# Performance work log

Measured on AMD Instinct MI355X. Metric: run time of the kernel, lower is better.

Reference implementation:

```python
import jax, jax.numpy as jnp
import numpy as np

DIM = 512
WH, WW = 8, 8
N = WH * WW  # 64 tokens per window
HEADS = 16
HEAD_DIM = DIM // HEADS
SCALE = HEAD_DIM ** -0.5
B_ = 2048
NW = 64  # number of distinct window masks; B_ % NW == 0


def _relative_position_index():
    coords = np.stack(np.meshgrid(np.arange(WH), np.arange(WW), indexing='ij')).reshape(2, -1)  # (2, N)
    rel = coords[:, :, None] - coords[:, None, :]          # (2, N, N)
    rel = rel.transpose(1, 2, 0).astype(np.int64)          # (N, N, 2)
    rel[..., 0] += WH - 1
    rel[..., 1] += WW - 1
    rel[..., 0] *= 2 * WW - 1
    return jnp.asarray(rel.sum(-1))                        # (N, N) in [0, (2Wh-1)(2Ww-1))


def setup_inputs() -> dict:
    key = jax.random.key(0)
    ks = jax.random.split(key, 10)
    q = jax.random.normal(ks[0], (B_, N, DIM), dtype=jnp.float32)
    mask = jax.random.normal(ks[1], (NW, N, N), dtype=jnp.float32)
    s = 0.02
    q_w = jax.random.normal(ks[2], (DIM, DIM), dtype=jnp.float32) * s
    q_b = jnp.zeros((DIM,), dtype=jnp.float32)
    kv_w = jax.random.normal(ks[3], (2 * DIM, DIM), dtype=jnp.float32) * s
    kv_b = jnp.zeros((2 * DIM,), dtype=jnp.float32)
    proj_w = jax.random.normal(ks[4], (DIM, DIM), dtype=jnp.float32) * s
    proj_b = jnp.zeros((DIM,), dtype=jnp.float32)
    bias_table = jax.random.normal(ks[5], ((2 * WH - 1) * (2 * WW - 1), HEADS), dtype=jnp.float32) * s
    rel_index = _relative_position_index()
    return {
        'q': q, 'mask': mask,
        'q_w': q_w, 'q_b': q_b, 'kv_w': kv_w, 'kv_b': kv_b,
        'proj_w': proj_w, 'proj_b': proj_b,
        'bias_table': bias_table, 'rel_index': rel_index,
    }


def reference(q, mask, q_w, q_b, kv_w, kv_b, proj_w, proj_b, bias_table, rel_index):
    Bn, n, c = q.shape
    # q/kv projections (torch Linear: x @ W.T + b)
    qh = (q @ q_w.T + q_b).reshape(Bn, n, HEADS, HEAD_DIM)
    kvh = (q @ kv_w.T + kv_b).reshape(Bn, n, 2, HEADS, HEAD_DIM)
    k = kvh[:, :, 0]  # (B_, N, H, hd)
    v = kvh[:, :, 1]
    # attention scores (B_, H, N, N)
    attn = jnp.einsum('bqhd,bkhd->bhqk', qh * SCALE, k)
    # relative position bias: gather (N*N, H) -> (H, N, N)
    bias = bias_table[rel_index.reshape(-1)].reshape(n, n, HEADS).transpose(2, 0, 1)
    attn = attn + bias[None]
    # shifted-window mask: (nW, N, N) broadcast over batch groups and heads
    nW = mask.shape[0]
    attn = attn.reshape(Bn // nW, nW, HEADS, n, n) + mask[None, :, None]
    attn = attn.reshape(Bn, HEADS, n, n)
    attn = jax.nn.softmax(attn, axis=-1)
    x = jnp.einsum('bhqk,bkhd->bqhd', attn, v).reshape(Bn, n, c)
    x = x @ proj_w.T + proj_b
    return (x, attn)
```

## Files before the change

kernel.cpp:

```cpp
#include <hip/hip_runtime.h>
#include <cstdint>
#include <cstddef>


typedef __bf16 bf16x8 __attribute__((ext_vector_type(8)));
typedef float  f32x4  __attribute__((ext_vector_type(4)));

#define MFMA16(a, b, c) __builtin_amdgcn_mfma_f32_16x16x32_bf16(a, b, c, 0, 0, 0)

__device__ __forceinline__ unsigned short f2bf(float f) {
  unsigned u = __float_as_uint(f);
  u += 0x7fffu + ((u >> 16) & 1u);
  return (unsigned short)(u >> 16);
}

__device__ __forceinline__ void gl2lds16(const void* g, void* l) {
  __builtin_amdgcn_global_load_lds(
      (const __attribute__((address_space(1))) void*)g,
      (__attribute__((address_space(3))) void*)l, 16, 0, 0);
}


__global__ __launch_bounds__(256) void cast_q_k(const float* __restrict__ src,
                                                unsigned short* __restrict__ dst) {
  long idx = (long)blockIdx.x * 256 + threadIdx.x;
  const float4* p = (const float4*)(src + idx * 8);
  float4 a = p[0], b = p[1];
  ushort4 r0 = make_ushort4(f2bf(a.x), f2bf(a.y), f2bf(a.z), f2bf(a.w));
  ushort4 r1 = make_ushort4(f2bf(b.x), f2bf(b.y), f2bf(b.z), f2bf(b.w));
  ushort4* o = (ushort4*)(dst + idx * 8);
  o[0] = r0; o[1] = r1;
}

__global__ __launch_bounds__(256) void pack_w_k(const float* __restrict__ qw,
                                                const float* __restrict__ kvw,
                                                const float* __restrict__ pwsrc,
                                                unsigned short* __restrict__ Wc,
                                                unsigned short* __restrict__ pw,
                                                float scale) {
  int idx = blockIdx.x * 256 + threadIdx.x;
  const float* src;
  unsigned short* dst;
  float s = 1.0f;
  if (idx < 98304) {
    long e = (long)idx * 8;
    int row = (int)(e >> 9);
    int k = (int)(e & 511);
    if (row < 512) { src = qw + (long)row * 512 + k; s = scale; }
    else           { src = kvw + (long)(row - 512) * 512 + k; }
    dst = Wc + e;
  } else {
    long e = (long)(idx - 98304) * 8;
    src = pwsrc + e;
    dst = pw + e;
  }
  float4 a = ((const float4*)src)[0];
  float4 b = ((const float4*)src)[1];
  ushort4 r0 = make_ushort4(f2bf(a.x * s), f2bf(a.y * s), f2bf(a.z * s), f2bf(a.w * s));
  ushort4 r1 = make_ushort4(f2bf(b.x * s), f2bf(b.y * s), f2bf(b.z * s), f2bf(b.w * s));
  ((ushort4*)dst)[0] = r0;
  ((ushort4*)dst)[1] = r1;
}

__global__ __launch_bounds__(256) void prep_misc_k(const float* __restrict__ btab,
                                                   const int* __restrict__ rel,
                                                   const float* __restrict__ qb,
                                                   const float* __restrict__ kvb,
                                                   float* __restrict__ biasF,
                                                   float* __restrict__ bc,
                                                   float scale) {
  int idx = blockIdx.x * 256 + threadIdx.x;
  if (idx < 65536) {
    int ij = idx & 4095;
    int h = idx >> 12;
    biasF[idx] = btab[rel[ij] * 16 + h];
  } else {
    int i = idx - 65536;
    bc[i] = (i < 512) ? qb[i] * scale : kvb[i - 512];
  }
}

template <bool BF16OUT>
__global__ __launch_bounds__(256) void gemm_bt(const unsigned short* __restrict__ A,
                                               const unsigned short* __restrict__ B,
                                               const float* __restrict__ bias,
                                               void* __restrict__ Cp, int N) {
  __shared__ unsigned short As[128 * 64];
  __shared__ unsigned short Bs[128 * 64];
  const int t = threadIdx.x;
  const int lane = t & 63;
  const int wave = t >> 6;
  const int wm = wave >> 1, wn = wave & 1;
  const int quad = lane >> 4, col = lane & 15;
  const long m0 = (long)blockIdx.x * 128;
  const long n0 = (long)blockIdx.y * 128;

  int sidx[4];
  long ga[4], gb[4];
#pragma unroll
  for (int i = 0; i < 4; ++i) {
    int idx = i * 256 + t;
    int r = idx >> 3, cl = idx & 7;
    int cg = cl ^ (r & 7);
    sidx[i] = idx * 8;
    ga[i] = (m0 + r) * 512 + cg * 8;
    gb[i] = (n0 + r) * 512 + cg * 8;
  }

  int offA[2][4], offB[2][4];
#pragma unroll
  for (int mt = 0; mt < 4; ++mt) {
    int rA = wm * 64 + mt * 16 + col;
    int rB = wn * 64 + mt * 16 + col;
#pragma unroll
    for (int ks = 0; ks < 2; ++ks) {
      offA[ks][mt] = rA * 64 + (((ks * 4 + quad) ^ (rA & 7)) * 8);
      offB[ks][mt] = rB * 64 + (((ks * 4 + quad) ^ (rB & 7)) * 8);
    }
  }

  f32x4 acc[4][4];
#pragma unroll
  for (int i = 0; i < 4; ++i)
#pragma unroll
    for (int j = 0; j < 4; ++j) acc[i][j] = (f32x4){0.f, 0.f, 0.f, 0.f};

  for (int kt = 0; kt < 8; ++kt) {
    const unsigned short* Ak = A + kt * 64;
    const unsigned short* Bk = B + kt * 64;
#pragma unroll
    for (int i = 0; i < 4; ++i) gl2lds16(Ak + ga[i], &As[sidx[i]]);
#pragma unroll
    for (int i = 0; i < 4; ++i) gl2lds16(Bk + gb[i], &Bs[sidx[i]]);
    asm volatile("s_waitcnt vmcnt(0)" ::: "memory");
    __syncthreads();
#pragma unroll
    for (int ks = 0; ks < 2; ++ks) {
      bf16x8 af[4], bf[4];
#pragma unroll
      for (int mt = 0; mt < 4; ++mt) af[mt] = *(const bf16x8*)&As[offA[ks][mt]];
#pragma unroll
      for (int nt = 0; nt < 4; ++nt) bf[nt] = *(const bf16x8*)&Bs[offB[ks][nt]];
#pragma unroll
      for (int mt = 0; mt < 4; ++mt)
#pragma unroll
        for (int nt = 0; nt < 4; ++nt)
          acc[mt][nt] = MFMA16(af[mt], bf[nt], acc[mt][nt]);
    }
    __syncthreads();
  }

#pragma unroll
  for (int nt = 0; nt < 4; ++nt) {
    long n = n0 + wn * 64 + nt * 16 + col;
    float bv = bias[n];
#pragma unroll
    for (int mt = 0; mt < 4; ++mt) {
      long mbase = m0 + wm * 64 + mt * 16 + quad * 4;
#pragma unroll
      for (int r = 0; r < 4; ++r) {
        float v = acc[mt][nt][r] + bv;
        long off = (mbase + r) * N + n;
        if (BF16OUT) ((unsigned short*)Cp)[off] = f2bf(v);
        else         ((float*)Cp)[off] = v;
      }
    }
  }
}

__global__ __launch_bounds__(64) void attn_k(const unsigned short* __restrict__ QKV,
                                             const float* __restrict__ mask,
                                             const float* __restrict__ biasF,
                                             float* __restrict__ attn_out,
                                             unsigned short* __restrict__ xh) {
  __shared__ unsigned short Plds[64 * 72];
  __shared__ unsigned short Vt[32 * 72];
  const int bh = blockIdx.x;
  const int b = bh >> 4, h = bh & 15;
  const int lane = threadIdx.x;
  const int quad = lane >> 4, col = lane & 15;
  const unsigned short* base = QKV + (long)b * 64 * 1536 + h * 32;

  {
    const unsigned short* vrow = base + 1024 + (long)lane * 1536;
#pragma unroll
    for (int c = 0; c < 4; ++c) {
      uint4 v = *(const uint4*)(vrow + c * 8);
      unsigned short* p = &Vt[(c * 8) * 72 + lane];
      p[0 * 72] = (unsigned short)(v.x);
      p[1 * 72] = (unsigned short)(v.x >> 16);
      p[2 * 72] = (unsigned short)(v.y);
      p[3 * 72] = (unsigned short)(v.y >> 16);
      p[4 * 72] = (unsigned short)(v.z);
      p[5 * 72] = (unsigned short)(v.z >> 16);
      p[6 * 72] = (unsigned short)(v.w);
      p[7 * 72] = (unsigned short)(v.w >> 16);
    }
  }

  bf16x8 qf[4], kf[4];
#pragma unroll
  for (int mt = 0; mt < 4; ++mt)
    qf[mt] = *(const bf16x8*)(base + (long)(mt * 16 + col) * 1536 + quad * 8);
#pragma unroll
  for (int nt = 0; nt < 4; ++nt)
    kf[nt] = *(const bf16x8*)(base + 512 + (long)(nt * 16 + col) * 1536 + quad * 8);

  const f32x4 z = (f32x4){0.f, 0.f, 0.f, 0.f};
  f32x4 s[4][4];
#pragma unroll
  for (int mt = 0; mt < 4; ++mt)
#pragma unroll
    for (int nt = 0; nt < 4; ++nt)
      s[mt][nt] = MFMA16(qf[mt], kf[nt], z);

  const float* mrow = mask + (long)(b & 63) * 4096;
  const float* brow = biasF + (long)h * 4096;
#pragma unroll
  for (int mt = 0; mt < 4; ++mt)
#pragma unroll
    for (int r = 0; r < 4; ++r) {
      int i = mt * 16 + quad * 4 + r;
#pragma unroll
      for (int nt = 0; nt < 4; ++nt) {
        int j = nt * 16 + col;
        s[mt][nt][r] += mrow[i * 64 + j] + brow[i * 64 + j];
      }
    }

  float inv[4][4];
#pragma unroll
  for (int mt = 0; mt < 4; ++mt)
#pragma unroll
    for (int r = 0; r < 4; ++r) {
      float m = fmaxf(fmaxf(s[mt][0][r], s[mt][1][r]), fmaxf(s[mt][2][r], s[mt][3][r]));
      m = fmaxf(m, __shfl_xor(m, 1));
      m = fmaxf(m, __shfl_xor(m, 2));
      m = fmaxf(m, __shfl_xor(m, 4));
      m = fmaxf(m, __shfl_xor(m, 8));
      float sum = 0.f;
#pragma unroll
      for (int nt = 0; nt < 4; ++nt) {
        float p = __expf(s[mt][nt][r] - m);
        s[mt][nt][r] = p;
        sum += p;
      }
      sum += __shfl_xor(sum, 1);
      sum += __shfl_xor(sum, 2);
      sum += __shfl_xor(sum, 4);
      sum += __shfl_xor(sum, 8);
      inv[mt][r] = 1.0f / sum;
    }

  float* aout = attn_out + (long)bh * 4096;
#pragma unroll
  for (int mt = 0; mt < 4; ++mt)
#pragma unroll
    for (int r = 0; r < 4; ++r) {
      int i = mt * 16 + quad * 4 + r;
      float iv = inv[mt][r];
#pragma unroll
      for (int nt = 0; nt < 4; ++nt) {
        int j = nt * 16 + col;
        float p = s[mt][nt][r] * iv;
        aout[i * 64 + j] = p;
        Plds[i * 72 + j] = f2bf(p);
      }
    }
  __syncthreads();

  f32x4 o[4][2];
#pragma unroll
  for (int mt = 0; mt < 4; ++mt)
#pragma unroll
    for (int n2 = 0; n2 < 2; ++n2) o[mt][n2] = z;
#pragma unroll
  for (int ks = 0; ks < 2; ++ks) {
    bf16x8 pa[4], vb[2];
#pragma unroll
    for (int mt = 0; mt < 4; ++mt)
      pa[mt] = *(const bf16x8*)&Plds[(mt * 16 + col) * 72 + ks * 32 + quad * 8];
#pragma unroll
    for (int n2 = 0; n2 < 2; ++n2)
      vb[n2] = *(const bf16x8*)&Vt[(n2 * 16 + col) * 72 + ks * 32 + quad * 8];
#pragma unroll
    for (int mt = 0; mt < 4; ++mt)
#pragma unroll
      for (int n2 = 0; n2 < 2; ++n2)
        o[mt][n2] = MFMA16(pa[mt], vb[n2], o[mt][n2]);
  }

  unsigned short* xrow = xh + (long)b * 64 * 512 + h * 32;
#pragma unroll
  for (int mt = 0; mt < 4; ++mt)
#pragma unroll
    for (int n2 = 0; n2 < 2; ++n2)
#pragma unroll
      for (int r = 0; r < 4; ++r) {
        int i = mt * 16 + quad * 4 + r;
        int d = n2 * 16 + col;
        xrow[(long)i * 512 + d] = f2bf(o[mt][n2][r]);
      }
}

extern "C" void kernel_launch(void* const* d_in, const int* in_sizes, int n_in,
                              void* d_out, int out_size, void* d_ws, size_t ws_size,
                              hipStream_t stream) {
  const float* q      = (const float*)d_in[0];
  const float* mask   = (const float*)d_in[1];
  const float* q_w    = (const float*)d_in[2];
  const float* q_b    = (const float*)d_in[3];
  const float* kv_w   = (const float*)d_in[4];
  const float* kv_b   = (const float*)d_in[5];
  const float* proj_w = (const float*)d_in[6];
  const float* proj_b = (const float*)d_in[7];
  const float* btab   = (const float*)d_in[8];
  const int*   rel    = (const int*)d_in[9];

  char* ws = (char*)d_ws;
  unsigned short* Aq    = (unsigned short*)ws;
  unsigned short* QKV   = (unsigned short*)(ws + 134217728LL);
  unsigned short* Wc    = (unsigned short*)(ws + 536870912LL);
  float*          bc    = (float*)(ws + 538443776LL);
  unsigned short* pw    = (unsigned short*)(ws + 538449920LL);
  float*          biasF = (float*)(ws + 538974208LL);
  unsigned short* xh    = Aq;

  float* x_out = (float*)d_out;
  float* attn_out = x_out + 67108864LL;

  const float scale = 0.17677669529663687f;

  cast_q_k<<<32768, 256, 0, stream>>>(q, Aq);
  pack_w_k<<<512, 256, 0, stream>>>(q_w, kv_w, proj_w, Wc, pw, scale);
  prep_misc_k<<<262, 256, 0, stream>>>(btab, rel, q_b, kv_b, biasF, bc, scale);
  gemm_bt<true><<<dim3(1024, 12), 256, 0, stream>>>(Aq, Wc, bc, (void*)QKV, 1536);
  attn_k<<<32768, 64, 0, stream>>>(QKV, mask, biasF, attn_out, xh);
  gemm_bt<false><<<dim3(1024, 4), 256, 0, stream>>>(xh, pw, proj_b, (void*)x_out, 512);
}
```

Measured before the change: 1.698 ms.

## Rewrite GEMM as 256x256 tile with double-buffered LDS ping-pong pipeline

The bf16 GEMM used for the QKV and output projections now uses 256x256 block tiles with 8 waves. Global-to-LDS loads for the next k-slice are interleaved with MFMA phases, using explicit barriers, partial vmcnt waits and raised wave priority around the MFMA bursts. This is meant to hide global load latency and raise arithmetic intensity per LDS byte compared with the previous load-wait-compute loop. The 128KB of LDS limits occupancy to one block per CU, and the kernel relies on hand-coded waitcnt counts being correct.

```diff
diff --git a/kernel.cpp b/kernel.cpp
--- a/kernel.cpp
+++ b/kernel.cpp
@@ -80,92 +80,132 @@
   }
 }
 
+
+#define BAR()   asm volatile("s_barrier" ::: "memory")
+#define LGKM0() asm volatile("s_waitcnt lgkmcnt(0)" ::: "memory")
+#define VMW(n)  asm volatile("s_waitcnt vmcnt(" #n ")" ::: "memory")
+
 template <bool BF16OUT>
-__global__ __launch_bounds__(256) void gemm_bt(const unsigned short* __restrict__ A,
-                                               const unsigned short* __restrict__ B,
-                                               const float* __restrict__ bias,
-                                               void* __restrict__ Cp, int N) {
-  __shared__ unsigned short As[128 * 64];
-  __shared__ unsigned short Bs[128 * 64];
+__global__ __launch_bounds__(512, 2) void gemm_bt(const unsigned short* __restrict__ A,
+                                                  const unsigned short* __restrict__ B,
+                                                  const float* __restrict__ bias,
+                                                  void* __restrict__ Cp, int N) {
+  __shared__ unsigned short Ls[2][2][256 * 64];
   const int t = threadIdx.x;
   const int lane = t & 63;
   const int wave = t >> 6;
-  const int wm = wave >> 1, wn = wave & 1;
+  const int wm = wave >> 2;
+  const int wn = wave & 3;
   const int quad = lane >> 4, col = lane & 15;
-  const long m0 = (long)blockIdx.x * 128;
-  const long n0 = (long)blockIdx.y * 128;
-
-  int sidx[4];
-  long ga[4], gb[4];
-#pragma unroll
-  for (int i = 0; i < 4; ++i) {
-    int idx = i * 256 + t;
-    int r = idx >> 3, cl = idx & 7;
-    int cg = cl ^ (r & 7);
-    sidx[i] = idx * 8;
-    ga[i] = (m0 + r) * 512 + cg * 8;
-    gb[i] = (n0 + r) * 512 + cg * 8;
-  }
-
-  int offA[2][4], offB[2][4];
-#pragma unroll
-  for (int mt = 0; mt < 4; ++mt) {
-    int rA = wm * 64 + mt * 16 + col;
-    int rB = wn * 64 + mt * 16 + col;
-#pragma unroll
-    for (int ks = 0; ks < 2; ++ks) {
-      offA[ks][mt] = rA * 64 + (((ks * 4 + quad) ^ (rA & 7)) * 8);
-      offB[ks][mt] = rB * 64 + (((ks * 4 + quad) ^ (rB & 7)) * 8);
-    }
-  }
-
-  f32x4 acc[4][4];
-#pragma unroll
-  for (int i = 0; i < 4; ++i)
+  const long m0 = (long)blockIdx.x * 256;
+  const long n0 = (long)blockIdx.y * 256;
+
+  int sL[2];
+  long gA[2], gB[2];
+#pragma unroll
+  for (int i = 0; i < 2; ++i) {
+    int idx = i * 512 + t;
+    int row = idx >> 3, cl = idx & 7;
+    int cg = cl ^ (row & 7);
+    sL[i] = idx * 8;
+    gA[i] = (m0 + row) * 512 + cg * 8;
+    gB[i] = (n0 + row) * 512 + cg * 8;
+  }
+
+#define ST_A(buf, h, kt) { \
+  gl2lds16(A + gA[0] + (long)(h) * 65536 + (long)(kt) * 64, &Ls[buf][0][(h) * 8192 + sL[0]]); \
+  gl2lds16(A + gA[1] + (long)(h) * 65536 + (long)(kt) * 64, &Ls[buf][0][(h) * 8192 + sL[1]]); }
+#define ST_B(buf, h, kt) { \
+  gl2lds16(B + gB[0] + (long)(h) * 65536 + (long)(kt) * 64, &Ls[buf][1][(h) * 8192 + sL[0]]); \
+  gl2lds16(B + gB[1] + (long)(h) * 65536 + (long)(kt) * 64, &Ls[buf][1][(h) * 8192 + sL[1]]); }
+
+  const int cks0 = (quad ^ (col & 7)) * 8;
+  const int cks1 = ((4 + quad) ^ (col & 7)) * 8;
+  int rAoff[2][4], rBoff[2][2];
+#pragma unroll
+  for (int m4 = 0; m4 < 4; ++m4) {
+    int rr = wm * 64 + m4 * 16 + col;
+    rAoff[0][m4] = rr * 64;
+    rAoff[1][m4] = (rr + 128) * 64;
+  }
+#pragma unroll
+  for (int n2 = 0; n2 < 2; ++n2) {
+    int rr = wn * 32 + n2 * 16 + col;
+    rBoff[0][n2] = rr * 64;
+    rBoff[1][n2] = (rr + 128) * 64;
+  }
+
+  bf16x8 a[4][2], b0[2][2], b1[2][2];
+  f32x4 acc[8][4];
+#pragma unroll
+  for (int i = 0; i < 8; ++i)
 #pragma unroll
     for (int j = 0; j < 4; ++j) acc[i][j] = (f32x4){0.f, 0.f, 0.f, 0.f};
 
-  for (int kt = 0; kt < 8; ++kt) {
-    const unsigned short* Ak = A + kt * 64;
-    const unsigned short* Bk = B + kt * 64;
-#pragma unroll
-    for (int i = 0; i < 4; ++i) gl2lds16(Ak + ga[i], &As[sidx[i]]);
-#pragma unroll
-    for (int i = 0; i < 4; ++i) gl2lds16(Bk + gb[i], &Bs[sidx[i]]);
-    asm volatile("s_waitcnt vmcnt(0)" ::: "memory");
-    __syncthreads();
-#pragma unroll
-    for (int ks = 0; ks < 2; ++ks) {
-      bf16x8 af[4], bf[4];
-#pragma unroll
-      for (int mt = 0; mt < 4; ++mt) af[mt] = *(const bf16x8*)&As[offA[ks][mt]];
-#pragma unroll
-      for (int nt = 0; nt < 4; ++nt) bf[nt] = *(const bf16x8*)&Bs[offB[ks][nt]];
-#pragma unroll
-      for (int mt = 0; mt < 4; ++mt)
-#pragma unroll
-        for (int nt = 0; nt < 4; ++nt)
-          acc[mt][nt] = MFMA16(af[mt], bf[nt], acc[mt][nt]);
-    }
-    __syncthreads();
-  }
-
-#pragma unroll
-  for (int nt = 0; nt < 4; ++nt) {
-    long n = n0 + wn * 64 + nt * 16 + col;
+#define RDA(buf, mh) { _Pragma("unroll") for (int m4 = 0; m4 < 4; ++m4) { \
+    a[m4][0] = *(const bf16x8*)&Ls[buf][0][rAoff[mh][m4] + cks0]; \
+    a[m4][1] = *(const bf16x8*)&Ls[buf][0][rAoff[mh][m4] + cks1]; } }
+#define RDB(buf, nh, breg) { _Pragma("unroll") for (int n2 = 0; n2 < 2; ++n2) { \
+    breg[n2][0] = *(const bf16x8*)&Ls[buf][1][rBoff[nh][n2] + cks0]; \
+    breg[n2][1] = *(const bf16x8*)&Ls[buf][1][rBoff[nh][n2] + cks1]; } }
+#define MM(mh, nh, breg) { __builtin_amdgcn_s_setprio(1); \
+  _Pragma("unroll") for (int m4 = 0; m4 < 4; ++m4) \
+  _Pragma("unroll") for (int n2 = 0; n2 < 2; ++n2) { \
+    acc[(mh) * 4 + m4][(nh) * 2 + n2] = \
+        MFMA16(a[m4][0], breg[n2][0], acc[(mh) * 4 + m4][(nh) * 2 + n2]); \
+    acc[(mh) * 4 + m4][(nh) * 2 + n2] = \
+        MFMA16(a[m4][1], breg[n2][1], acc[(mh) * 4 + m4][(nh) * 2 + n2]); } \
+  __builtin_amdgcn_s_setprio(0); }
+
+#define ITER(it, LAST) { \
+  const int kt1 = 2 * (it) + 1; \
+   RDA(0, 0); RDB(0, 0, b0); ST_A(1, 1, kt1); \
+           BAR(); LGKM0(); MM(0, 0, b0); BAR(); \
+   RDB(0, 1, b1); if (!(LAST)) { ST_A(0, 0, kt1 + 1); } \
+           BAR(); LGKM0(); MM(0, 1, b1); BAR(); \
+   RDA(0, 1); if (!(LAST)) { ST_B(0, 0, kt1 + 1); } \
+           BAR(); LGKM0(); MM(1, 1, b1); BAR(); \
+   if (!(LAST)) { ST_B(0, 1, kt1 + 1); VMW(6); } else { VMW(0); } \
+           BAR(); LGKM0(); MM(1, 0, b0); BAR(); \
+   RDA(1, 0); RDB(1, 0, b0); if (!(LAST)) { ST_A(0, 1, kt1 + 1); } \
+           BAR(); LGKM0(); MM(0, 0, b0); BAR(); \
+   RDB(1, 1, b1); if (!(LAST)) { ST_A(1, 0, kt1 + 2); } \
+           BAR(); LGKM0(); MM(0, 1, b1); BAR(); \
+   RDA(1, 1); if (!(LAST)) { ST_B(1, 0, kt1 + 2); } \
+           BAR(); LGKM0(); MM(1, 1, b1); BAR(); \
+   if (!(LAST)) { ST_B(1, 1, kt1 + 2); VMW(6); } \
+           BAR(); LGKM0(); MM(1, 0, b0); BAR(); \
+}
+
+  ST_A(0, 0, 0); ST_B(0, 0, 0); ST_B(0, 1, 0); ST_A(0, 1, 0);
+  ST_A(1, 0, 1); ST_B(1, 0, 1); ST_B(1, 1, 1);
+  VMW(6); BAR();
+
+  for (int it = 0; it < 3; ++it) { ITER(it, 0); }
+  ITER(3, 1);
+
+#pragma unroll
+  for (int ni = 0; ni < 4; ++ni) {
+    long n = n0 + (ni >> 1) * 128 + wn * 32 + (ni & 1) * 16 + col;
     float bv = bias[n];
 #pragma unroll
-    for (int mt = 0; mt < 4; ++mt) {
-      long mbase = m0 + wm * 64 + mt * 16 + quad * 4;
+    for (int mi = 0; mi < 8; ++mi) {
+      long mb = m0 + (mi >> 2) * 128 + wm * 64 + (mi & 3) * 16 + quad * 4;
 #pragma unroll
       for (int r = 0; r < 4; ++r) {
-        float v = acc[mt][nt][r] + bv;
-        long off = (mbase + r) * N + n;
+        float v = acc[mi][ni][r] + bv;
+        long off = (mb + r) * N + n;
         if (BF16OUT) ((unsigned short*)Cp)[off] = f2bf(v);
         else         ((float*)Cp)[off] = v;
       }
     }
   }
+#undef ST_A
+#undef ST_B
+#undef RDA
+#undef RDB
+#undef MM
+#undef ITER
 }
 
 __global__ __launch_bounds__(64) void attn_k(const unsigned short* __restrict__ QKV,
@@ -334,7 +374,7 @@
   cast_q_k<<<32768, 256, 0, stream>>>(q, Aq);
   pack_w_k<<<512, 256, 0, stream>>>(q_w, kv_w, proj_w, Wc, pw, scale);
   prep_misc_k<<<262, 256, 0, stream>>>(btab, rel, q_b, kv_b, biasF, bc, scale);
-  gemm_bt<true><<<dim3(1024, 12), 256, 0, stream>>>(Aq, Wc, bc, (void*)QKV, 1536);
+  gemm_bt<true><<<dim3(512, 6), 512, 0, stream>>>(Aq, Wc, bc, (void*)QKV, 1536);
   attn_k<<<32768, 64, 0, stream>>>(QKV, mask, biasF, attn_out, xh);
-  gemm_bt<false><<<dim3(1024, 4), 256, 0, stream>>>(xh, pw, proj_b, (void*)x_out, 512);
-}
+  gemm_bt<false><<<dim3(512, 2), 512, 0, stream>>>(xh, pw, proj_b, (void*)x_out, 512);
+}
```

New measurement: 1.619 ms. 1.05x faster.
